# Performance work log

Measured on AMD Instinct MI355X. Metric: run time of the kernel, lower is better.

## Reference

```python
import jax, jax.numpy as jnp
import numpy as np

B, F = 32, 8192
GRAVITY = 9.81007
GYRO_COV = 0.0032 ** 2   # per-axis gyroscope noise covariance
ACC_COV = 0.08 ** 2      # per-axis accelerometer noise covariance


def _skew(v):
    # v: (..., 3) -> (..., 3, 3) skew-symmetric (hat) matrix
    x, y, z = v[..., 0], v[..., 1], v[..., 2]
    o = jnp.zeros_like(x)
    return jnp.stack([
        jnp.stack([o, -z, y], -1),
        jnp.stack([z, o, -x], -1),
        jnp.stack([-y, x, o], -1)], -2)


def _qmul(a, b):
    # Hamilton product, xyzw convention (pypose layout): a (x) b
    ax, ay, az, aw = a[..., 0], a[..., 1], a[..., 2], a[..., 3]
    bx, by, bz, bw = b[..., 0], b[..., 1], b[..., 2], b[..., 3]
    return jnp.stack([
        aw * bx + ax * bw + ay * bz - az * by,
        aw * by - ax * bz + ay * bw + az * bx,
        aw * bz + ax * by - ay * bx + az * bw,
        aw * bw - ax * bx - ay * by - az * bz], -1)


def _so3_exp_quat(phi):
    # so3 exponential map -> unit quaternion (xyzw), numerically safe near 0
    th2 = jnp.sum(phi * phi, -1, keepdims=True)
    small = th2 < 1e-8
    th = jnp.sqrt(jnp.where(small, 1.0, th2))
    s = jnp.where(small, 0.5 - th2 / 48.0, jnp.sin(0.5 * th) / th)
    w = jnp.where(small, 1.0 - th2 / 8.0, jnp.cos(0.5 * th))
    return jnp.concatenate([phi * s, w], -1)


def _quat_to_mat(q):
    # unit quaternion (xyzw) -> rotation matrix (..., 3, 3)
    x, y, z, w = q[..., 0], q[..., 1], q[..., 2], q[..., 3]
    r0 = jnp.stack([1 - 2 * (y * y + z * z), 2 * (x * y - z * w), 2 * (x * z + y * w)], -1)
    r1 = jnp.stack([2 * (x * y + z * w), 1 - 2 * (x * x + z * z), 2 * (y * z - x * w)], -1)
    r2 = jnp.stack([2 * (x * z - y * w), 2 * (y * z + x * w), 1 - 2 * (x * x + y * y)], -1)
    return jnp.stack([r0, r1, r2], -2)


def _so3_Jr(phi):
    # Right Jacobian of SO3: Jr = I - c1*K + c2*K^2, safe near 0
    th2 = jnp.sum(phi * phi, -1)[..., None, None]
    small = th2 < 1e-8
    th2s = jnp.where(small, 1.0, th2)
    th = jnp.sqrt(th2s)
    c1 = jnp.where(small, 0.5 - th2 / 24.0, (1.0 - jnp.cos(th)) / th2s)
    c2 = jnp.where(small, 1.0 / 6.0 - th2 / 120.0, (th - jnp.sin(th)) / (th2s * th))
    K = _skew(phi)
    I = jnp.eye(3, dtype=phi.dtype)
    return I - c1 * K + c2 * (K @ K)


def setup_inputs() -> dict:
    key = jax.random.key(0)
    k1, k2, k3 = jax.random.split(key, 3)
    dt = jax.random.uniform(k1, (B, F, 1), dtype=jnp.float32) * 0.004 + 0.001
    gyro = jax.random.normal(k2, (B, F, 3), dtype=jnp.float32)
    acc = jax.random.normal(k3, (B, F, 3), dtype=jnp.float32)
    pos0 = jnp.zeros((B, 3), dtype=jnp.float32)
    vel0 = jnp.zeros((B, 3), dtype=jnp.float32)
    return {"dt": dt, "gyro": gyro, "acc": acc, "pos0": pos0, "vel0": vel0}


def _preintegrate(dt, gyro, acc, pos0, vel0):
    dtype = acc.dtype
    g = jnp.array([0.0, 0.0, GRAVITY], dtype=dtype)
    I3 = jnp.eye(3, dtype=dtype)

    # --- rotation integration: dR_{k+1} = dR_k Exp(w_k dt_k) ---
    w = gyro * dt                                             # (B,F,3)
    dq = _so3_exp_quat(w)                                     # (B,F,4) per-step increments
    incre_q = jax.lax.associative_scan(_qmul, dq, axis=1)     # cumprod q0 (x) ... (x) qk
    R_incl = _quat_to_mat(incre_q)                            # (B,F,3,3) inclusive DeltaR_{ik+1}
    R_pre = jnp.concatenate(
        [jnp.broadcast_to(I3, (R_incl.shape[0], 1, 3, 3)), R_incl[:, :-1]], axis=1)  # DeltaR_{ik}

    # gravity removed in body frame: a_k = acc_k - R_k^{-1} g  (R^{-1} g = R^T g)
    a = acc - jnp.einsum('bfji,j->bfi', R_incl, g)            # (B,F,3)

    # --- velocity / position integration ---
    dv_step = jnp.einsum('bfij,bfj->bfi', R_pre, a) * dt      # DeltaR_{ik} a_k dt
    dvel = jnp.cumsum(dv_step, axis=1)                        # Delta v
    vel = vel0[:, None, :] + dvel
    dvel_prev = jnp.concatenate([jnp.zeros_like(dvel[:, :1]), dvel[:, :-1]], axis=1)
    dpos = jnp.cumsum(dvel_prev * dt + 0.5 * dv_step * dt, axis=1)
    pos = pos0[:, None, :] + dpos

    # --- covariance propagation: C' = A C A^T + Bg Cg Bg^T + Ba Ca Ba^T ---
    Bn, Fn = dt.shape[0], dt.shape[1]
    dRT = jnp.swapaxes(_quat_to_mat(dq), -1, -2)              # Exp(w dt)^T
    Ra = jnp.einsum('bfij,bfjk->bfik', R_pre, _skew(a))       # DeltaR (a^)
    dt1 = dt[..., None]                                       # (B,F,1,1)

    A = jnp.zeros((Bn, Fn, 9, 9), dtype=dtype)
    A = A.at[..., 0:3, 0:3].set(dRT)
    A = A.at[..., 3:6, 0:3].set(-Ra * dt1)
    A = A.at[..., 6:9, 0:3].set(-0.5 * Ra * dt1 * dt1)
    A = A.at[..., 3:6, 3:6].set(I3)
    A = A.at[..., 6:9, 6:9].set(I3)
    A = A.at[..., 6:9, 3:6].set(I3 * dt1)

    qg = jnp.full((3,), GYRO_COV, dtype=dtype)
    qa = jnp.full((3,), ACC_COV, dtype=dtype)
    Bg = _so3_Jr(w) * dt1                                     # (B,F,3,3)
    Bv = R_pre * dt1
    Bp = 0.5 * R_pre * dt1 * dt1
    Ngg = jnp.einsum('bfik,k,bfjk->bfij', Bg, qg, Bg)
    Nvv = jnp.einsum('bfik,k,bfjk->bfij', Bv, qa, Bv)
    Nvp = jnp.einsum('bfik,k,bfjk->bfij', Bv, qa, Bp)
    Npp = jnp.einsum('bfik,k,bfjk->bfij', Bp, qa, Bp)
    N = jnp.zeros((Bn, Fn, 9, 9), dtype=dtype)
    N = N.at[..., 0:3, 0:3].set(Ngg)
    N = N.at[..., 3:6, 3:6].set(Nvv)
    N = N.at[..., 3:6, 6:9].set(Nvp)
    N = N.at[..., 6:9, 3:6].set(jnp.swapaxes(Nvp, -1, -2))
    N = N.at[..., 6:9, 6:9].set(Npp)

    def step(C, AN):
        Ak, Nk = AN
        C = jnp.einsum('bij,bjk,blk->bil', Ak, C, Ak) + Nk
        return C, None

    C0 = jnp.zeros((Bn, 9, 9), dtype=dtype)
    cov, _ = jax.lax.scan(step, C0, (jnp.moveaxis(A, 1, 0), jnp.moveaxis(N, 1, 0)))

    # init rot is identity -> output rot equals the incremental cumprod
    return incre_q, vel, pos, cov


def reference(dt, gyro, acc, pos0, vel0):
    return _preintegrate(dt, gyro, acc, pos0, vel0)
```

## Files before the change

### kernel.cpp

```cpp
#include <hip/hip_runtime.h>


#define BB 32
#define FF 8192
#define NCH 128
#define SLOT 64
#define GRAV 9.81007f
#define GCOV (0.0032f*0.0032f)
#define ACOV (0.08f*0.08f)

#define COV_OFF  0
#define QTOT_OFF 262144
#define QPRE_OFF 278528
#define VP_OFF   294912

struct Quat { float x, y, z, w; };

__device__ __forceinline__ Quat qmul(const Quat a, const Quat b) {
    Quat r;
    r.x = a.w*b.x + a.x*b.w + a.y*b.z - a.z*b.y;
    r.y = a.w*b.y - a.x*b.z + a.y*b.w + a.z*b.x;
    r.z = a.w*b.z + a.x*b.y - a.y*b.x + a.z*b.w;
    r.w = a.w*b.w - a.x*b.x - a.y*b.y - a.z*b.z;
    return r;
}

__device__ __forceinline__ Quat qshfl_up(const Quat a, int s) {
    Quat r;
    r.x=__shfl_up(a.x,s); r.y=__shfl_up(a.y,s);
    r.z=__shfl_up(a.z,s); r.w=__shfl_up(a.w,s);
    return r;
}

__device__ __forceinline__ Quat qexp3(float px, float py, float pz) {
    float th2 = px*px + py*py + pz*pz;
    float s = 0.5f - th2 * (1.0f/48.0f);
    float w = 1.0f - th2 * 0.125f;
    Quat q; q.x=px*s; q.y=py*s; q.z=pz*s; q.w=w; return q;
}

__device__ __forceinline__ void quat2mat(const Quat q, float* R) {
    float x=q.x, y=q.y, z=q.z, w=q.w;
    R[0]=1.0f-2.0f*(y*y+z*z); R[1]=2.0f*(x*y-z*w);       R[2]=2.0f*(x*z+y*w);
    R[3]=2.0f*(x*y+z*w);      R[4]=1.0f-2.0f*(x*x+z*z);  R[5]=2.0f*(y*z-x*w);
    R[6]=2.0f*(x*z-y*w);      R[7]=2.0f*(y*z+x*w);       R[8]=1.0f-2.0f*(x*x+y*y);
}

__device__ __forceinline__ void mm_nn(const float* A, const float* B, float* C) {
#pragma unroll
    for (int i=0;i<3;i++)
#pragma unroll
    for (int j=0;j<3;j++)
        C[3*i+j] = A[3*i+0]*B[0+j] + A[3*i+1]*B[3+j] + A[3*i+2]*B[6+j];
}

__device__ __forceinline__ void mm_nt(const float* A, const float* B, float* C) {
#pragma unroll
    for (int i=0;i<3;i++)
#pragma unroll
    for (int j=0;j<3;j++)
        C[3*i+j] = A[3*i+0]*B[3*j+0] + A[3*i+1]*B[3*j+1] + A[3*i+2]*B[3*j+2];
}

__device__ __forceinline__ void mm_tn(const float* A, const float* B, float* C) {
#pragma unroll
    for (int i=0;i<3;i++)
#pragma unroll
    for (int j=0;j<3;j++)
        C[3*i+j] = A[0+i]*B[0+j] + A[3+i]*B[3+j] + A[6+i]*B[6+j];
}

__device__ __forceinline__ void mm_nt_sym(const float* A, const float* B, float* O6) {
    O6[0]=A[0]*B[0]+A[1]*B[1]+A[2]*B[2];
    O6[1]=A[0]*B[3]+A[1]*B[4]+A[2]*B[5];
    O6[2]=A[0]*B[6]+A[1]*B[7]+A[2]*B[8];
    O6[3]=A[3]*B[3]+A[4]*B[4]+A[5]*B[5];
    O6[4]=A[3]*B[6]+A[4]*B[7]+A[5]*B[8];
    O6[5]=A[6]*B[6]+A[7]*B[7]+A[8]*B[8];
}

__device__ __forceinline__ void mm_nn_sym(const float* A, const float* B, float* O6) {
    O6[0]=A[0]*B[0]+A[1]*B[3]+A[2]*B[6];
    O6[1]=A[0]*B[1]+A[1]*B[4]+A[2]*B[7];
    O6[2]=A[0]*B[2]+A[1]*B[5]+A[2]*B[8];
    O6[3]=A[3]*B[1]+A[4]*B[4]+A[5]*B[7];
    O6[4]=A[3]*B[2]+A[4]*B[5]+A[5]*B[8];
    O6[5]=A[6]*B[2]+A[7]*B[5]+A[8]*B[8];
}

__device__ __forceinline__ void expand_sym(const float* t, float* M) {
    M[0]=t[0]; M[1]=t[1]; M[2]=t[2];
    M[3]=t[1]; M[4]=t[3]; M[5]=t[4];
    M[6]=t[2]; M[7]=t[4]; M[8]=t[5];
}

__device__ __forceinline__ void m_skew(const float* M, float v0, float v1, float v2, float* C) {
#pragma unroll
    for (int i=0;i<3;i++) {
        C[3*i+0] = M[3*i+1]*v2 - M[3*i+2]*v1;
        C[3*i+1] = M[3*i+2]*v0 - M[3*i+0]*v2;
        C[3*i+2] = M[3*i+0]*v1 - M[3*i+1]*v0;
    }
}

__device__ __forceinline__ void skew_m(float w0, float w1, float w2, const float* M, float* C) {
#pragma unroll
    for (int j=0;j<3;j++) {
        C[0+j] = -w2*M[3+j] + w1*M[6+j];
        C[3+j] =  w2*M[0+j] - w0*M[6+j];
        C[6+j] = -w1*M[0+j] + w0*M[3+j];
    }
}

__global__ __launch_bounds__(256) void k_chunktot(
    const float* __restrict__ dt, const float* __restrict__ gyro,
    float* __restrict__ qtot, float* __restrict__ outq)
{
    const int bid=blockIdx.x, b=bid>>5, wg=bid&31;
    const int tid=threadIdx.x, lane=tid&63, wid=tid>>6;
    const int c=wg*4+wid;
    const long k=(long)b*FF+(long)c*64+lane;
    float d=dt[k];
    Quat inc=qexp3(gyro[3*k+0]*d, gyro[3*k+1]*d, gyro[3*k+2]*d);
#pragma unroll
    for (int s=1;s<64;s<<=1) {
        Quat p=qshfl_up(inc,s);
        if (lane>=s) inc=qmul(p,inc);
    }
    { float4 o; o.x=inc.x; o.y=inc.y; o.z=inc.z; o.w=inc.w;
      reinterpret_cast<float4*>(outq)[k]=o; }
    if (lane==63) {
        float4 o; o.x=inc.x; o.y=inc.y; o.z=inc.z; o.w=inc.w;
        reinterpret_cast<float4*>(qtot)[b*NCH+c]=o;
    }
}

__global__ __launch_bounds__(128) void k_qpre(
    const float* __restrict__ qtot, float* __restrict__ qpre)
{
    const int b=blockIdx.x, c=threadIdx.x, lane=c&63, w=c>>6;
    __shared__ float4 w0t;
    __shared__ float4 all[NCH];
    float4 t=reinterpret_cast<const float4*>(qtot)[b*NCH+c];
    Quat inc; inc.x=t.x; inc.y=t.y; inc.z=t.z; inc.w=t.w;
#pragma unroll
    for (int s=1;s<64;s<<=1) {
        Quat p=qshfl_up(inc,s);
        if (lane>=s) inc=qmul(p,inc);
    }
    if (w==0 && lane==63) { float4 o; o.x=inc.x;o.y=inc.y;o.z=inc.z;o.w=inc.w; w0t=o; }
    __syncthreads();
    if (w==1) { Quat p; p.x=w0t.x;p.y=w0t.y;p.z=w0t.z;p.w=w0t.w; inc=qmul(p,inc); }
    { float4 o; o.x=inc.x;o.y=inc.y;o.z=inc.z;o.w=inc.w; all[c]=o; }
    __syncthreads();
    float4 pre;
    if (c==0) { pre.x=0.f;pre.y=0.f;pre.z=0.f;pre.w=1.f; }
    else pre=all[c-1];
    reinterpret_cast<float4*>(qpre)[b*NCH+c]=pre;
}

#define RSTR 66
__global__ __launch_bounds__(256) void k_main(
    const float* __restrict__ dt, const float* __restrict__ gyro,
    const float* __restrict__ acc, const float* __restrict__ qpre_g,
    float* __restrict__ outq, float* __restrict__ cov, float* __restrict__ vp_g,
    float* __restrict__ outv, float* __restrict__ outp)
{
    __shared__ float red[4][23][RSTR];
    const int bid=blockIdx.x, b=bid>>5, wg=bid&31;
    const int tid=threadIdx.x, lane=tid&63, wid=tid>>6;
    const int c=wg*4+wid;
    const long k=(long)b*FF+(long)c*64+lane;

    const float d=dt[k];
    const float wx=gyro[3*k+0]*d, wy=gyro[3*k+1]*d, wz=gyro[3*k+2]*d;

    Quat qloc;
    { float4 t=reinterpret_cast<const float4*>(outq)[k];
      qloc.x=t.x; qloc.y=t.y; qloc.z=t.z; qloc.w=t.w; }
    float4 tp=reinterpret_cast<const float4*>(qpre_g)[b*NCH+c];
    Quat qpre; qpre.x=tp.x; qpre.y=tp.y; qpre.z=tp.z; qpre.w=tp.w;
    Quat qi=qmul(qpre,qloc);
    { float4 o; o.x=qi.x;o.y=qi.y;o.z=qi.z;o.w=qi.w;
      reinterpret_cast<float4*>(outq)[k]=o; }

    Quat ql1=qshfl_up(qloc,1);
    if (lane==0) { ql1.x=0.f; ql1.y=0.f; ql1.z=0.f; ql1.w=1.f; }
    Quat cq; cq.x=-ql1.x; cq.y=-ql1.y; cq.z=-ql1.z; cq.w=ql1.w;
    Quat dqq=qmul(cq,qloc);

    float a0=acc[3*k+0]-GRAV*2.0f*(qi.x*qi.z-qi.y*qi.w);
    float a1=acc[3*k+1]-GRAV*2.0f*(qi.y*qi.z+qi.x*qi.w);
    float a2=acc[3*k+2]-GRAV*(1.0f-2.0f*(qi.x*qi.x+qi.y*qi.y));

    float Rl[9]; quat2mat(ql1,Rl);
    float b0=Rl[0]*a0+Rl[1]*a1+Rl[2]*a2;
    float b1=Rl[3]*a0+Rl[4]*a1+Rl[5]*a2;
    float b2=Rl[6]*a0+Rl[7]*a1+Rl[8]*a2;
    float m0=d*b0, m1=d*b1, m2=d*b2;

    float td=d, M0=m0, M1=m1, M2=m2;
#pragma unroll
    for (int s=1;s<64;s<<=1) {
        float p3=__shfl_up(td,s), p0=__shfl_up(M0,s), p1=__shfl_up(M1,s), p2=__shfl_up(M2,s);
        if (lane>=s) { td+=p3; M0+=p0; M1+=p1; M2+=p2; }
    }
    float Dtot=__shfl(td,63);
    float tau = Dtot - td;
    float cn = 0.5f*d + tau;
    float n0=cn*m0, n1=cn*m1, n2=cn*m2;
    float N0=n0, N1=n1, N2=n2;
#pragma unroll
    for (int s=1;s<64;s<<=1) {
        float p0=__shfl_up(N0,s),p1=__shfl_up(N1,s),p2=__shfl_up(N2,s);
        if (lane>=s){ N0+=p0; N1+=p1; N2+=p2; }
    }
    float u0=(M0-0.5f*m0)*d, u1=(M1-0.5f*m1)*d, u2=(M2-0.5f*m2)*d;
    float U0=u0, U1=u1, U2=u2;
#pragma unroll
    for (int s=1;s<64;s<<=1) {
        float p0=__shfl_up(U0,s),p1=__shfl_up(U1,s),p2=__shfl_up(U2,s);
        if (lane>=s){ U0+=p0; U1+=p1; U2+=p2; }
    }
    float Mt0=__shfl(M0,63), Mt1=__shfl(M1,63), Mt2=__shfl(M2,63);
    float Nt0=__shfl(N0,63), Nt1=__shfl(N1,63), Nt2=__shfl(N2,63);
    float mp0=Mt0-M0, mp1=Mt1-M1, mp2=Mt2-M2;
    float np0=Nt0-N0, np1=Nt1-N1, np2=Nt2-N2;

    float Rp9[9]; quat2mat(qpre,Rp9);
    float pv0=Rp9[0]*M0+Rp9[1]*M1+Rp9[2]*M2;
    float pv1=Rp9[3]*M0+Rp9[4]*M1+Rp9[5]*M2;
    float pv2=Rp9[6]*M0+Rp9[7]*M1+Rp9[8]*M2;
    float pp0=Rp9[0]*U0+Rp9[1]*U1+Rp9[2]*U2;
    float pp1=Rp9[3]*U0+Rp9[4]*U1+Rp9[5]*U2;
    float pp2=Rp9[6]*U0+Rp9[7]*U1+Rp9[8]*U2;
    outv[3*k+0]=pv0; outv[3*k+1]=pv1; outv[3*k+2]=pv2;
    outp[3*k+0]=pp0; outp[3*k+1]=pp1; outp[3*k+2]=pp2;

    const long wsbase=((long)b*NCH+c)*SLOT;
    if (lane==63) {
        float4* vp4=reinterpret_cast<float4*>(vp_g+(long)(b*NCH+c)*8);
        float4 v0; v0.x=pv0; v0.y=pv1; v0.z=pv2; v0.w=pp0;
        float4 v1; v1.x=pp1; v1.y=pp2; v1.z=td;  v1.w=0.f;
        vp4[0]=v0; vp4[1]=v1;
        float4* pw=reinterpret_cast<float4*>(cov+wsbase+48);
        float4 w0; w0.x=qloc.x; w0.y=qloc.y; w0.z=qloc.z; w0.w=qloc.w;
        float4 w1; w1.x=qpre.x; w1.y=qpre.y; w1.z=qpre.z; w1.w=qpre.w;
        float4 w2; w2.x=M0; w2.y=M1; w2.z=M2; w2.w=N0;
        float4 w3; w3.x=N1; w3.y=N2; w3.z=td; w3.w=0.f;
        pw[0]=w0; pw[1]=w1; pw[2]=w2; pw[3]=w3;
    }

    float th2 = wx*wx + wy*wy + wz*wz;
    float c1, c2;
    if (th2 < 1e-8f) { c1 = 0.5f - th2*(1.0f/24.0f); c2 = (1.0f/6.0f) - th2*(1.0f/120.0f); }
    else {
        float s2q = dqq.x*dqq.x + dqq.y*dqq.y + dqq.z*dqq.z;
        c1 = 2.0f*s2q/th2;
        float th = sqrtf(th2);
        float snt = 2.0f*sqrtf(s2q)*dqq.w;
        c2 = (th - snt)/(th2*th);
    }
    float J[9];
    {
        float dg = 1.0f - c2*th2;
        J[0]=dg + c2*wx*wx;      J[1]= c1*wz + c2*wx*wy;  J[2]=-c1*wy + c2*wx*wz;
        J[3]=-c1*wz + c2*wx*wy;  J[4]=dg + c2*wy*wy;      J[5]= c1*wx + c2*wy*wz;
        J[6]= c1*wy + c2*wx*wz;  J[7]=-c1*wx + c2*wy*wz;  J[8]=dg + c2*wz*wz;
    }
    float Rj[9]; quat2mat(qloc,Rj);
    float H[9]; mm_nn(Rj,J,H);
    const float gs = GCOV*d*d;
    float Gp[9];
    Gp[0]=gs*(H[0]*H[0]+H[1]*H[1]+H[2]*H[2]);
    Gp[1]=gs*(H[0]*H[3]+H[1]*H[4]+H[2]*H[5]);
    Gp[2]=gs*(H[0]*H[6]+H[1]*H[7]+H[2]*H[8]);
    Gp[4]=gs*(H[3]*H[3]+H[4]*H[4]+H[5]*H[5]);
    Gp[5]=gs*(H[3]*H[6]+H[4]*H[7]+H[5]*H[8]);
    Gp[8]=gs*(H[6]*H[6]+H[7]*H[7]+H[8]*H[8]);
    Gp[3]=Gp[1]; Gp[6]=Gp[2]; Gp[7]=Gp[5];

    const float av  = ACOV*d*d;
    const float bv  = 0.5f*ACOV*d*d*d;
    const float cv  = 0.25f*ACOV*d*d*d*d;
    const float vpd = av*tau + bv;
    const float ppd = av*tau*tau + 2.0f*bv*tau + cv;

    float Crv[9], Crp[9], Cvv[9], Cvp[9], Cpp[9];
    m_skew(Gp, mp0,mp1,mp2, Crv);
    m_skew(Gp, np0,np1,np2, Crp);
    skew_m(-mp0,-mp1,-mp2, Crv, Cvv);
    skew_m(-mp0,-mp1,-mp2, Crp, Cvp);
    skew_m(-np0,-np1,-np2, Crp, Cpp);

    float S45[45];
#pragma unroll
    for (int i=0;i<9;i++){ S45[i]=Crv[i]; S45[9+i]=Crp[i]; S45[18+i]=Cvp[i]; }
    S45[18]+=vpd; S45[22]+=vpd; S45[26]+=vpd;
    S45[27]=Gp[0];  S45[28]=Gp[1];  S45[29]=Gp[2];  S45[30]=Gp[4];  S45[31]=Gp[5];  S45[32]=Gp[8];
    S45[33]=Cvv[0]+av; S45[34]=Cvv[1]; S45[35]=Cvv[2]; S45[36]=Cvv[4]+av; S45[37]=Cvv[5]; S45[38]=Cvv[8]+av;
    S45[39]=Cpp[0]+ppd; S45[40]=Cpp[1]; S45[41]=Cpp[2]; S45[42]=Cpp[4]+ppd; S45[43]=Cpp[5]; S45[44]=Cpp[8]+ppd;

#pragma unroll
    for (int e=0;e<23;e++) red[wid][e][lane] = S45[e];
    __syncthreads();
    float r1 = 0.f;
    if (lane < 23) {
        const float* row = &red[wid][lane][0];
        float ax=0.f, ay=0.f;
#pragma unroll
        for (int i=0;i<32;i++) {
            float2 v = reinterpret_cast<const float2*>(row)[i];
            ax += v.x; ay += v.y;
        }
        r1 = ax + ay;
    }
    __syncthreads();
#pragma unroll
    for (int e=0;e<22;e++) red[wid][e][lane] = S45[23+e];
    __syncthreads();
    float r2 = 0.f;
    if (lane < 22) {
        const float* row = &red[wid][lane][0];
        float ax=0.f, ay=0.f;
#pragma unroll
        for (int i=0;i<32;i++) {
            float2 v = reinterpret_cast<const float2*>(row)[i];
            ax += v.x; ay += v.y;
        }
        r2 = ax + ay;
    }
    if (lane < 23) cov[wsbase+lane] = r1;
    if (lane < 22) cov[wsbase+23+lane] = r2;
}

__device__ __forceinline__ void congr45(const float* Phi, const float* S, float* O)
{
    const float* D=Phi; const float* P=Phi+9; const float* Q=Phi+18; const float T=Phi[27];
    const float* Arv=S+0; const float* Arp=S+9; const float* Avp=S+18;
    float Arr[9], Avv[9], App[9];
    expand_sym(S+27,Arr); expand_sym(S+33,Avv); expand_sym(S+39,App);

    float M1[9], M2[9], M3[9], t1[9], t6[6];
    mm_nn(D,Arr,M1); mm_nn(D,Arv,M2); mm_nn(D,Arp,M3);
    mm_nt_sym(M1, D, O+27);
    mm_nt(M1, P, t1);
#pragma unroll
    for (int i=0;i<9;i++) O[0+i] = t1[i] + M2[i];
    mm_nt(M1, Q, t1);
#pragma unroll
    for (int i=0;i<9;i++) O[9+i] = t1[i] + T*M2[i] + M3[i];

    float W1[9], W2[9], W3[9];
    mm_nn(P, Arr, W1);
#pragma unroll
    for (int i=0;i<3;i++)
#pragma unroll
    for (int j=0;j<3;j++) W1[3*i+j] += Arv[3*j+i];
    mm_nn(P, Arv, W2);
#pragma unroll
    for (int i=0;i<9;i++) W2[i] += Avv[i];
    mm_nn(P, Arp, W3);
#pragma unroll
    for (int i=0;i<9;i++) W3[i] += Avp[i];
    mm_nt_sym(W1, P, t6);
    O[33+0]=t6[0]+W2[0]; O[33+1]=t6[1]+W2[1]; O[33+2]=t6[2]+W2[2];
    O[33+3]=t6[3]+W2[4]; O[33+4]=t6[4]+W2[5]; O[33+5]=t6[5]+W2[8];
    mm_nt(W1, Q, t1);
#pragma unroll
    for (int i=0;i<9;i++) O[18+i] = t1[i] + T*W2[i] + W3[i];

    float U1[9], U2[9], U3[9];
    mm_nn(Q, Arr, U1);
#pragma unroll
    for (int i=0;i<3;i++)
#pragma unroll
    for (int j=0;j<3;j++) U1[3*i+j] += T*Arv[3*j+i] + Arp[3*j+i];
    mm_nn(Q, Arv, U2);
#pragma unroll
    for (int i=0;i<3;i++)
#pragma unroll
    for (int j=0;j<3;j++) U2[3*i+j] += T*Avv[3*i+j] + Avp[3*j+i];
    mm_nn(Q, Arp, U3);
#pragma unroll
    for (int i=0;i<9;i++) U3[i] += T*Avp[i] + App[i];
    mm_nt_sym(U1, Q, t6);
    O[39+0]=t6[0]+T*U2[0]+U3[0]; O[39+1]=t6[1]+T*U2[1]+U3[1]; O[39+2]=t6[2]+T*U2[2]+U3[2];
    O[39+3]=t6[3]+T*U2[4]+U3[4]; O[39+4]=t6[4]+T*U2[5]+U3[5]; O[39+5]=t6[5]+T*U2[8]+U3[8];
}

__global__ __launch_bounds__(256) void k_merged(
    const float* __restrict__ dt, const float* __restrict__ pos0,
    const float* __restrict__ vel0, const float* __restrict__ vp_g,
    const float* __restrict__ cov,
    float* __restrict__ outv, float* __restrict__ outp, float* __restrict__ outc)
{
    __shared__ float sc[NCH][13];
    __shared__ float hand[12];
    __shared__ float wsum[2][45];
    const int bid=blockIdx.x;
    const int tid=threadIdx.x, lane=tid&63, wid=tid>>6;

    if (bid < BB) {
        const int b = bid;
        const bool own = tid < NCH;
        const float* g = cov + (long)b*NCH*SLOT + (long)tid*SLOT;

        float qt0=0.f,qt1=0.f,qt2=0.f,qt3=1.f, qp0=0.f,qp1=0.f,qp2=0.f,qp3=1.f;
        float q0,q1,q2,q3, Mv0,Mv1,Mv2, Nv0,Nv1,Nv2, Tv;
        if (own) {
            const float4* pr=reinterpret_cast<const float4*>(g+48);
            float4 r0=pr[0], r1=pr[1], r2=pr[2], r3=pr[3];
            qt0=r0.x; qt1=r0.y; qt2=r0.z; qt3=r0.w;
            qp0=r1.x; qp1=r1.y; qp2=r1.z; qp3=r1.w;
            Mv0=r2.x; Mv1=r2.y; Mv2=r2.z;
            Nv0=r2.w; Nv1=r3.x; Nv2=r3.y;
            Tv=r3.z;
            q0=qt0; q1=qt1; q2=qt2; q3=qt3;
        } else { q0=q1=q2=0.f; q3=1.f; Mv0=Mv1=Mv2=Nv0=Nv1=Nv2=0.f; Tv=0.f; }

        if (own) {
#pragma unroll
            for (int s=1;s<64;s<<=1) {
                float a0=__shfl_down(q0,s), a1=__shfl_down(q1,s), a2=__shfl_down(q2,s), a3=__shfl_down(q3,s);
                float am0=__shfl_down(Mv0,s), am1=__shfl_down(Mv1,s), am2=__shfl_down(Mv2,s);
                float an0=__shfl_down(Nv0,s), an1=__shfl_down(Nv1,s), an2=__shfl_down(Nv2,s);
                float aT=__shfl_down(Tv,s);
                if (lane+s < 64) {
                    Quat qb; qb.x=q0; qb.y=q1; qb.z=q2; qb.w=q3;
                    Quat qa; qa.x=a0; qa.y=a1; qa.z=a2; qa.w=a3;
                    Quat qc=qmul(qb,qa);
                    float Rb[9]; quat2mat(qb,Rb);
                    float Mc0=Mv0+Rb[0]*am0+Rb[1]*am1+Rb[2]*am2;
                    float Mc1=Mv1+Rb[3]*am0+Rb[4]*am1+Rb[5]*am2;
                    float Mc2=Mv2+Rb[6]*am0+Rb[7]*am1+Rb[8]*am2;
                    float Nc0=Nv0+Rb[0]*an0+Rb[1]*an1+Rb[2]*an2+aT*Mv0;
                    float Nc1=Nv1+Rb[3]*an0+Rb[4]*an1+Rb[5]*an2+aT*Mv1;
                    float Nc2=Nv2+Rb[6]*an0+Rb[7]*an1+Rb[8]*an2+aT*Mv2;
                    q0=qc.x; q1=qc.y; q2=qc.z; q3=qc.w;
                    Mv0=Mc0; Mv1=Mc1; Mv2=Mc2;
                    Nv0=Nc0; Nv1=Nc1; Nv2=Nc2;
                    Tv+=aT;
                }
            }
            if (wid==1 && lane==0) {
                hand[0]=q0; hand[1]=q1; hand[2]=q2; hand[3]=q3;
                hand[4]=Mv0; hand[5]=Mv1; hand[6]=Mv2;
                hand[7]=Nv0; hand[8]=Nv1; hand[9]=Nv2;
                hand[10]=Tv;
            }
        }
        __syncthreads();
        if (own && wid==0) {
            Quat qb; qb.x=q0; qb.y=q1; qb.z=q2; qb.w=q3;
            Quat qa; qa.x=hand[0]; qa.y=hand[1]; qa.z=hand[2]; qa.w=hand[3];
            float am0=hand[4],am1=hand[5],am2=hand[6];
            float an0=hand[7],an1=hand[8],an2=hand[9];
            float aT=hand[10];
            Quat qc=qmul(qb,qa);
            float Rb[9]; quat2mat(qb,Rb);
            float Mc0=Mv0+Rb[0]*am0+Rb[1]*am1+Rb[2]*am2;
            float Mc1=Mv1+Rb[3]*am0+Rb[4]*am1+Rb[5]*am2;
            float Mc2=Mv2+Rb[6]*am0+Rb[7]*am1+Rb[8]*am2;
            float Nc0=Nv0+Rb[0]*an0+Rb[1]*an1+Rb[2]*an2+aT*Mv0;
            float Nc1=Nv1+Rb[3]*an0+Rb[4]*an1+Rb[5]*an2+aT*Mv1;
            float Nc2=Nv2+Rb[6]*an0+Rb[7]*an1+Rb[8]*an2+aT*Mv2;
            q0=qc.x; q1=qc.y; q2=qc.z; q3=qc.w;
            Mv0=Mc0; Mv1=Mc1; Mv2=Mc2;
            Nv0=Nc0; Nv1=Nc1; Nv2=Nc2;
            Tv+=aT;
        }
        if (own) {
            sc[tid][0]=q0; sc[tid][1]=q1; sc[tid][2]=q2; sc[tid][3]=q3;
            sc[tid][4]=Mv0; sc[tid][5]=Mv1; sc[tid][6]=Mv2;
            sc[tid][7]=Nv0; sc[tid][8]=Nv1; sc[tid][9]=Nv2;
            sc[tid][10]=Tv;
        }
        __syncthreads();

        float O[45];
        if (own) {
            Quat qt; qt.x=qt0; qt.y=qt1; qt.z=qt2; qt.w=qt3;
            Quat qp; qp.x=qp0; qp.y=qp1; qp.z=qp2; qp.w=qp3;

            float Phi[28];
            if (tid < NCH-1) {
                Quat qs; qs.x=sc[tid+1][0]; qs.y=sc[tid+1][1]; qs.z=sc[tid+1][2]; qs.w=sc[tid+1][3];
                float Ms0=sc[tid+1][4], Ms1=sc[tid+1][5], Ms2=sc[tid+1][6];
                float Ns0=sc[tid+1][7], Ns1=sc[tid+1][8], Ns2=sc[tid+1][9];
                float Ts=sc[tid+1][10];
                float Rs[9]; quat2mat(qs,Rs);
                Phi[0]=Rs[0]; Phi[1]=Rs[3]; Phi[2]=Rs[6];
                Phi[3]=Rs[1]; Phi[4]=Rs[4]; Phi[5]=Rs[7];
                Phi[6]=Rs[2]; Phi[7]=Rs[5]; Phi[8]=Rs[8];
                Quat qp1=qmul(qp,qt);
                float Rp1[9]; quat2mat(qp1,Rp1);
                float Pc[9]; m_skew(Rp1, -Ms0,-Ms1,-Ms2, Pc);
                float Qc[9]; m_skew(Rp1, -Ns0,-Ns1,-Ns2, Qc);
#pragma unroll
                for (int i=0;i<9;i++){ Phi[9+i]=Pc[i]; Phi[18+i]=Qc[i]; }
                Phi[27]=Ts;
            } else {
#pragma unroll
                for (int i=0;i<9;i++){ Phi[i]=(i%4==0)?1.f:0.f; Phi[9+i]=0.f; Phi[18+i]=0.f; }
                Phi[27]=0.f;
            }

            float Rt[9]; quat2mat(qt,Rt);
            float Rp[9]; quat2mat(qp,Rp);
            float S[45];
            {
                float Crv[9],Crp[9],Cvp9[9], e9[9], t9[9], o9[9], o6[6];
#pragma unroll
                for (int i=0;i<9;i++){ Crv[i]=g[i]; Crp[i]=g[9+i]; Cvp9[i]=g[18+i]; }
                mm_tn(Rt, Crv, t9); mm_nt(t9, Rp, o9);
#pragma unroll
                for (int i=0;i<9;i++) S[i]=o9[i];
                mm_tn(Rt, Crp, t9); mm_nt(t9, Rp, o9);
#pragma unroll
                for (int i=0;i<9;i++) S[9+i]=o9[i];
                mm_nn(Rp, Cvp9, t9); mm_nt(t9, Rp, o9);
#pragma unroll
                for (int i=0;i<9;i++) S[18+i]=o9[i];
                expand_sym(g+27, e9); mm_tn(Rt, e9, t9); mm_nn_sym(t9, Rt, o6);
#pragma unroll
                for (int i=0;i<6;i++) S[27+i]=o6[i];
                expand_sym(g+33, e9); mm_nn(Rp, e9, t9); mm_nt_sym(t9, Rp, o6);
#pragma unroll
                for (int i=0;i<6;i++) S[33+i]=o6[i];
                expand_sym(g+39, e9); mm_nn(Rp, e9, t9); mm_nt_sym(t9, Rp, o6);
#pragma unroll
                for (int i=0;i<6;i++) S[39+i]=o6[i];
            }
            congr45(Phi, S, O);

#pragma unroll
            for (int m=1;m<64;m<<=1) {
#pragma unroll
                for (int i=0;i<45;i++) O[i] += __shfl_xor(O[i], m);
            }
            if (lane==0) {
#pragma unroll
                for (int i=0;i<45;i++) wsum[wid][i] = O[i];
            }
        }
        __syncthreads();

        if (tid < 81) {
            int i = tid/9, j = tid%9;
            int bi = i/3, ii = i%3, bj = j/3, jj = j%3;
            int lo = (ii<jj)?ii:jj, hi = (ii<jj)?jj:ii;
            int tix = (lo==0)?hi:((lo==1)?(2+hi):5);
            int x;
            if      (bi==0 && bj==0) x = 27 + tix;
            else if (bi==0 && bj==1) x = 0  + 3*ii + jj;
            else if (bi==0 && bj==2) x = 9  + 3*ii + jj;
            else if (bi==1 && bj==0) x = 0  + 3*jj + ii;
            else if (bi==1 && bj==1) x = 33 + tix;
            else if (bi==1 && bj==2) x = 18 + 3*ii + jj;
            else if (bi==2 && bj==0) x = 9  + 3*jj + ii;
            else if (bi==2 && bj==1) x = 18 + 3*jj + ii;
            else                     x = 39 + tix;
            outc[(long)b*81 + tid] = wsum[0][x] + wsum[1][x];
        }
        return;
    }

    const int ebid = bid - BB;
    const int b = ebid>>5, wg = ebid&31;
    const int c = wg*4+wid;
    const long k = (long)b*FF+(long)c*64+lane;

    const float4* vpb = reinterpret_cast<const float4*>(vp_g + (long)b*NCH*8);
    float4 A0=vpb[4*lane+0], A1=vpb[4*lane+1];
    float4 B0=vpb[4*lane+2], B1=vpb[4*lane+3];

    float pl0=A0.x+B0.x, pl1=A0.y+B0.y, pl2=A0.z+B0.z;
    float i0=pl0,i1=pl1,i2=pl2;
#pragma unroll
    for (int s=1;s<64;s<<=1) {
        float p0=__shfl_up(i0,s),p1=__shfl_up(i1,s),p2=__shfl_up(i2,s);
        if (lane>=s){ i0+=p0; i1+=p1; i2+=p2; }
    }
    float e0V0=i0-pl0, e0V1=i1-pl1, e0V2=i2-pl2;
    float e1V0=e0V0+A0.x, e1V1=e0V1+A0.y, e1V2=e0V2+A0.z;
    float u00=e0V0*A1.z+A0.w, u01=e0V1*A1.z+A1.x, u02=e0V2*A1.z+A1.y;
    float u10=e1V0*B1.z+B0.w, u11=e1V1*B1.z+B1.x, u12=e1V2*B1.z+B1.y;
    float pu0=u00+u10, pu1=u01+u11, pu2=u02+u12;
    float j0=pu0,j1=pu1,j2=pu2;
#pragma unroll
    for (int s=1;s<64;s<<=1) {
        float p0=__shfl_up(j0,s),p1=__shfl_up(j1,s),p2=__shfl_up(j2,s);
        if (lane>=s){ j0+=p0; j1+=p1; j2+=p2; }
    }
    float e0P0=j0-pu0, e0P1=j1-pu1, e0P2=j2-pu2;
    float e1P0=e0P0+u00, e1P1=e0P1+u01, e1P2=e0P2+u02;

    const int srcl = c>>1;
    float sV0=(c&1)? e1V0:e0V0, sV1=(c&1)? e1V1:e0V1, sV2=(c&1)? e1V2:e0V2;
    float sP0=(c&1)? e1P0:e0P0, sP1=(c&1)? e1P1:e0P1, sP2=(c&1)? e1P2:e0P2;
    float V0=__shfl(sV0,srcl), V1=__shfl(sV1,srcl), V2=__shfl(sV2,srcl);
    float P0=__shfl(sP0,srcl), P1=__shfl(sP1,srcl), P2=__shfl(sP2,srcl);

    float td = dt[k];
#pragma unroll
    for (int s=1;s<64;s<<=1) {
        float p=__shfl_up(td,s);
        if (lane>=s) td+=p;
    }

    float v0x=vel0[3*b+0], v0y=vel0[3*b+1], v0z=vel0[3*b+2];
    float p0x=pos0[3*b+0], p0y=pos0[3*b+1], p0z=pos0[3*b+2];

    float pv0=outv[3*k+0], pv1=outv[3*k+1], pv2=outv[3*k+2];
    float pp0=outp[3*k+0], pp1=outp[3*k+1], pp2=outp[3*k+2];

    outv[3*k+0]=v0x+V0+pv0;
    outv[3*k+1]=v0y+V1+pv1;
    outv[3*k+2]=v0z+V2+pv2;
    outp[3*k+0]=p0x+P0+V0*td+pp0;
    outp[3*k+1]=p0y+P1+V1*td+pp1;
    outp[3*k+2]=p0z+P2+V2*td+pp2;
}

extern "C" void kernel_launch(void* const* d_in, const int* in_sizes, int n_in,
                              void* d_out, int out_size, void* d_ws, size_t ws_size,
                              hipStream_t stream)
{
    const float* dt   = (const float*)d_in[0];
    const float* gyro = (const float*)d_in[1];
    const float* acc  = (const float*)d_in[2];
    const float* pos0 = (const float*)d_in[3];
    const float* vel0 = (const float*)d_in[4];

    float* out  = (float*)d_out;
    float* outq = out;
    float* outv = out  + (long)BB*FF*4;
    float* outp = outv + (long)BB*FF*3;
    float* outc = outp + (long)BB*FF*3;

    float* ws   = (float*)d_ws;
    float* cov  = ws + COV_OFF;
    float* qtot = ws + QTOT_OFF;
    float* qpre = ws + QPRE_OFF;
    float* vp   = ws + VP_OFF;

    hipLaunchKernelGGL(k_chunktot, dim3(BB*32),    dim3(256), 0, stream, dt, gyro, qtot, outq);
    hipLaunchKernelGGL(k_qpre,     dim3(BB),       dim3(128), 0, stream, qtot, qpre);
    hipLaunchKernelGGL(k_main,     dim3(BB*32),    dim3(256), 0, stream, dt, gyro, acc, qpre, outq, cov, vp, outv, outp);
    hipLaunchKernelGGL(k_merged,   dim3(BB*32+BB), dim3(256), 0, stream, dt, pos0, vel0, vp, cov, outv, outp, outc);
}
```

Measured before the change: 33.02 us.

## Fuse chunk-prefix scan into chunktot via last-block atomic counter

Removes the separate k_qpre launch. Each block of k_chunktot now increments a per-batch atomic counter after writing its chunk totals, and the last of the 32 blocks for that batch runs the cross-chunk quaternion scan and writes qpre. This saves one kernel launch and its dependency gap, at the cost of threadfences and an atomic per block. It relies on a counter that is never reset, using a mod-32 check so repeated calls keep working.

Result: slower. 115.9 us (+251.1%).

```diff
diff --git a/kernel.cpp b/kernel.cpp
--- a/kernel.cpp
+++ b/kernel.cpp
@@ -13,6 +13,7 @@
 #define QTOT_OFF 262144
 #define QPRE_OFF 278528
 #define VP_OFF   294912
+#define CTR_OFF  327680
 
 struct Quat { float x, y, z, w; };
 
@@ -114,8 +115,12 @@
 
 __global__ __launch_bounds__(256) void k_chunktot(
     const float* __restrict__ dt, const float* __restrict__ gyro,
-    float* __restrict__ qtot, float* __restrict__ outq)
+    float* __restrict__ qtot, float* __restrict__ outq,
+    float* __restrict__ qpre, unsigned* __restrict__ ctr)
 {
+    __shared__ float4 all[NCH];
+    __shared__ float4 w0t;
+    __shared__ int trig;
     const int bid=blockIdx.x, b=bid>>5, wg=bid&31;
     const int tid=threadIdx.x, lane=tid&63, wid=tid>>6;
     const int c=wg*4+wid;
@@ -133,30 +138,42 @@
         float4 o; o.x=inc.x; o.y=inc.y; o.z=inc.z; o.w=inc.w;
         reinterpret_cast<float4*>(qtot)[b*NCH+c]=o;
     }
-}
-
-__global__ __launch_bounds__(128) void k_qpre(
-    const float* __restrict__ qtot, float* __restrict__ qpre)
-{
-    const int b=blockIdx.x, c=threadIdx.x, lane=c&63, w=c>>6;
-    __shared__ float4 w0t;
-    __shared__ float4 all[NCH];
-    float4 t=reinterpret_cast<const float4*>(qtot)[b*NCH+c];
-    Quat inc; inc.x=t.x; inc.y=t.y; inc.z=t.z; inc.w=t.w;
-#pragma unroll
-    for (int s=1;s<64;s<<=1) {
-        Quat p=qshfl_up(inc,s);
-        if (lane>=s) inc=qmul(p,inc);
-    }
-    if (w==0 && lane==63) { float4 o; o.x=inc.x;o.y=inc.y;o.z=inc.z;o.w=inc.w; w0t=o; }
+
+    __threadfence();
     __syncthreads();
-    if (w==1) { Quat p; p.x=w0t.x;p.y=w0t.y;p.z=w0t.z;p.w=w0t.w; inc=qmul(p,inc); }
-    { float4 o; o.x=inc.x;o.y=inc.y;o.z=inc.z;o.w=inc.w; all[c]=o; }
+    if (tid==0) {
+        unsigned old = atomicAdd(ctr + b, 1u);
+        trig = ((old & 31u) == 31u) ? 1 : 0;
+    }
     __syncthreads();
-    float4 pre;
-    if (c==0) { pre.x=0.f;pre.y=0.f;pre.z=0.f;pre.w=1.f; }
-    else pre=all[c-1];
-    reinterpret_cast<float4*>(qpre)[b*NCH+c]=pre;
+    if (!trig) return;
+    __threadfence();
+
+    Quat sq;
+    const int l2=tid&63, w2=tid>>6;
+    if (tid < NCH) {
+        float4 t=reinterpret_cast<const float4*>(qtot)[b*NCH+tid];
+        sq.x=t.x; sq.y=t.y; sq.z=t.z; sq.w=t.w;
+#pragma unroll
+        for (int s=1;s<64;s<<=1) {
+            Quat p=qshfl_up(sq,s);
+            if (l2>=s) sq=qmul(p,sq);
+        }
+        if (w2==0 && l2==63) { float4 o; o.x=sq.x;o.y=sq.y;o.z=sq.z;o.w=sq.w; w0t=o; }
+    }
+    __syncthreads();
+    if (tid>=64 && tid<NCH) {
+        Quat p; p.x=w0t.x;p.y=w0t.y;p.z=w0t.z;p.w=w0t.w;
+        sq=qmul(p,sq);
+    }
+    if (tid < NCH) { float4 o; o.x=sq.x;o.y=sq.y;o.z=sq.z;o.w=sq.w; all[tid]=o; }
+    __syncthreads();
+    if (tid < NCH) {
+        float4 pre;
+        if (tid==0) { pre.x=0.f;pre.y=0.f;pre.z=0.f;pre.w=1.f; }
+        else pre=all[tid-1];
+        reinterpret_cast<float4*>(qpre)[b*NCH+tid]=pre;
+    }
 }
 
 #define RSTR 66
@@ -644,9 +661,9 @@
     float* qtot = ws + QTOT_OFF;
     float* qpre = ws + QPRE_OFF;
     float* vp   = ws + VP_OFF;
-
-    hipLaunchKernelGGL(k_chunktot, dim3(BB*32),    dim3(256), 0, stream, dt, gyro, qtot, outq);
-    hipLaunchKernelGGL(k_qpre,     dim3(BB),       dim3(128), 0, stream, qtot, qpre);
+    unsigned* ctr = (unsigned*)(ws + CTR_OFF);
+
+    hipLaunchKernelGGL(k_chunktot, dim3(BB*32),    dim3(256), 0, stream, dt, gyro, qtot, outq, qpre, ctr);
     hipLaunchKernelGGL(k_main,     dim3(BB*32),    dim3(256), 0, stream, dt, gyro, acc, qpre, outq, cov, vp, outv, outp);
     hipLaunchKernelGGL(k_merged,   dim3(BB*32+BB), dim3(256), 0, stream, dt, pos0, vel0, vp, cov, outv, outp, outc);
 }
```
